# Kernel optimization log

Hardware: AMD Instinct MI355X
Metric: run time of the kernel (lower is better)

Reference implementation:

```python
import jax, jax.numpy as jnp
import numpy as np

BN_EPS = 1e-3  # Keras BatchNormalization default epsilon


def _conv_block(x, k):
    """Per-task conv (stride 2, pad 1) -> ReLU -> BatchNorm (center/scale=False, training).

    x: [B, E, H, W, Cin]  (B tasks, E examples per task)
    k: [B, kh, kw, Cin, Cout]  per-task kernel
    """
    def conv_one(xe, kt):  # xe: [E,H,W,Cin], kt: [kh,kw,Cin,Cout]
        return jax.lax.conv_general_dilated(
            xe, kt, window_strides=(2, 2), padding=[(1, 1), (1, 1)],
            dimension_numbers=('NHWC', 'HWIO', 'NHWC'))
    y = jax.nn.relu(jax.vmap(conv_one)(x, k))  # [B,E,H',W',Cout]
    # BatchNorm in training mode: moments over all axes except channels
    m = jnp.mean(y, axis=(0, 1, 2, 3))
    v = jnp.var(y, axis=(0, 1, 2, 3))
    return (y - m) * jax.lax.rsqrt(v + BN_EPS)


def setup_inputs() -> dict:
    key = jax.random.key(0)
    ks = jax.random.split(key, 6)
    B, E, H, C, O = 64, 64, 28, 64, 20
    return {
        'x': jax.random.normal(ks[0], (B, E, H, H, 1), dtype=jnp.float32),
        'k1': jax.random.normal(ks[1], (B, 3, 3, 1, C), dtype=jnp.float32) * 0.1,
        'k2': jax.random.normal(ks[2], (B, 3, 3, C, C), dtype=jnp.float32) * 0.05,
        'k3': jax.random.normal(ks[3], (B, 3, 3, C, C), dtype=jnp.float32) * 0.05,
        'k4': jax.random.normal(ks[4], (B, 3, 3, C, C), dtype=jnp.float32) * 0.05,
        'w_ro': jax.random.normal(ks[5], (B, C, O), dtype=jnp.float32) * 0.1,
    }


def reference(x, k1, k2, k3, k4, w_ro):
    h = _conv_block(x, k1)   # [B,E,14,14,C]
    h = _conv_block(h, k2)   # [B,E,7,7,C]
    h = _conv_block(h, k3)   # [B,E,4,4,C]
    h = _conv_block(h, k4)   # [B,E,2,2,C]
    # MaxPooling2D with pool size == full spatial extent -> global spatial max
    feat = jnp.max(h, axis=(2, 3))  # [B,E,C]
    # per-task readout matmul: [B,E,H] x [B,H,O] -> [B,E,O]
    return jnp.einsum('beh,bho->beo', feat, w_ro)
```

## Files before the change

### kernel.cpp

```cpp
#include <hip/hip_runtime.h>

#define BN_EPS 1e-3f

typedef __attribute__((ext_vector_type(8))) short bf16x8;
typedef __attribute__((ext_vector_type(16))) float floatx16;
typedef unsigned short u16;

__device__ __forceinline__ u16 f2bf(float f) {
  unsigned u = __float_as_uint(f);
  u += 0x7fffu + ((u >> 16) & 1u);
  return (u16)(u >> 16);
}
__device__ __forceinline__ float bf2f(u16 h) {
  return __uint_as_float(((unsigned)h) << 16);
}

static constexpr int NSHARD = 64;

__global__ __launch_bounds__(256) void conv1_k(
    const float* __restrict__ x, const float* __restrict__ k1,
    u16* __restrict__ y1, float* __restrict__ statsSh)
{
  __shared__ float xp[30 * 32];
  __shared__ float w1s[576];
  __shared__ float redsum[64], redss[64];

  const int be = blockIdx.x, b = be >> 6, tid = threadIdx.x;

  for (int i = tid; i < 960; i += 256) xp[i] = 0.f;
  for (int i = tid; i < 576; i += 256) w1s[i] = k1[(size_t)b * 576 + i];
  if (tid < 64) { redsum[tid] = 0.f; redss[tid] = 0.f; }
  __syncthreads();
  for (int i = tid; i < 784; i += 256) {
    const int r = i / 28, c = i - 28 * r;
    xp[(r + 1) * 32 + (c + 1)] = x[(size_t)be * 784 + i];
  }
  __syncthreads();

  if (tid < 224) {
    const int oy = tid >> 4, cg = (tid & 15) * 4;
    float w[4][9];
#pragma unroll
    for (int cc = 0; cc < 4; ++cc)
#pragma unroll
      for (int t = 0; t < 9; ++t) w[cc][t] = w1s[t * 64 + cg + cc];

    float xr[3][29];
#pragma unroll
    for (int ky = 0; ky < 3; ++ky)
#pragma unroll
      for (int j = 0; j < 29; ++j) xr[ky][j] = xp[(2 * oy + ky) * 32 + j];

    float sum[4] = {0.f, 0.f, 0.f, 0.f}, ss[4] = {0.f, 0.f, 0.f, 0.f};
#pragma unroll
    for (int ox = 0; ox < 14; ++ox) {
      alignas(8) u16 o[4];
#pragma unroll
      for (int cc = 0; cc < 4; ++cc) {
        float a = 0.f;
#pragma unroll
        for (int ky = 0; ky < 3; ++ky)
#pragma unroll
          for (int kx = 0; kx < 3; ++kx)
            a = fmaf(xr[ky][2 * ox + kx], w[cc][ky * 3 + kx], a);
        const float v = fmaxf(a, 0.f);
        o[cc] = f2bf(v);
        sum[cc] += v;
        ss[cc] = fmaf(v, v, ss[cc]);
      }
      *(uint2*)&y1[((size_t)be * 196 + oy * 14 + ox) * 64 + cg] = *(uint2*)o;
    }
#pragma unroll
    for (int cc = 0; cc < 4; ++cc) {
      atomicAdd(&redsum[cg + cc], sum[cc]);
      atomicAdd(&redss[cg + cc], ss[cc]);
    }
  }
  __syncthreads();
  if (tid < 64) {
    const int sh = be & (NSHARD - 1);
    atomicAdd(&statsSh[sh * 128 + tid], redsum[tid]);
    atomicAdd(&statsSh[sh * 128 + 64 + tid], redss[tid]);
  }
}

__global__ __launch_bounds__(256) void foldw_k(
    const float* __restrict__ W, const float* __restrict__ statsSh, float invN,
    u16* __restrict__ Wf, float* __restrict__ biasCls)
{
  __shared__ float T[64 * 68];
  __shared__ float P[256];
  __shared__ float s1[64], t1[64];
  __shared__ float tbS[64];

  const int b = blockIdx.x / 3, sg = blockIdx.x % 3;
  const int tid = threadIdx.x;

  {
    const int g = tid >> 7, cidx = tid & 127;
    float acc = 0.f;
    for (int k = 0; k < NSHARD / 2; ++k)
      acc += statsSh[(g * (NSHARD / 2) + k) * 128 + cidx];
    P[tid] = acc;
  }
  __syncthreads();
  if (tid < 64) {
    const float m = (P[tid] + P[tid + 128]) * invN;
    const float var = fmaf(-m, m, (P[64 + tid] + P[192 + tid]) * invN);
    const float s = rsqrtf(var + BN_EPS);
    s1[tid] = s;
    t1[tid] = -m * s;
  }
  __syncthreads();

  const int cin = tid >> 2, q0 = (tid & 3) * 16;
  const int cout = tid >> 2, ci0 = (tid & 3) * 16;
  for (int s = sg * 3; s < sg * 3 + 3; ++s) {
    if (tid < 64) tbS[tid] = 0.f;
    const float* ss = W + ((size_t)b * 9 + s) * 4096;
#pragma unroll
    for (int q = 0; q < 16; q += 4) {
      const float4 v = *(const float4*)(ss + cin * 64 + q0 + q);
      T[(q0 + q + 0) * 68 + cin] = v.x;
      T[(q0 + q + 1) * 68 + cin] = v.y;
      T[(q0 + q + 2) * 68 + cin] = v.z;
      T[(q0 + q + 3) * 68 + cin] = v.w;
    }
    __syncthreads();
    alignas(16) u16 tmp[16];
    float tb = 0.f;
#pragma unroll
    for (int j = 0; j < 16; ++j) {
      const float wv = T[cout * 68 + ci0 + j];
      tmp[j] = f2bf(wv * s1[ci0 + j]);
      tb = fmaf(t1[ci0 + j], wv, tb);
    }
    u16* dst = Wf + ((size_t)b * 9 + s) * 4096 + cout * 64 + ci0;
    *(uint4*)dst       = *(uint4*)&tmp[0];
    *(uint4*)(dst + 8) = *(uint4*)&tmp[8];
    atomicAdd(&tbS[cout], tb);
    __syncthreads();
    if (tid < 64) {
      const int ky = s / 3, kx = s % 3;
      const float tv = tbS[tid];
#pragma unroll
      for (int cls = 0; cls < 9; ++cls) {
        const int ry = cls / 3, rx = cls % 3;
        const bool valid = !((ry == 1 && ky == 0) || (ry == 2 && ky == 2) ||
                             (rx == 1 && kx == 0) || (rx == 2 && kx == 2));
        if (valid) atomicAdd(&biasCls[(size_t)b * 576 + cls * 64 + tid], tv);
      }
    }
    __syncthreads();
  }
}

template <int Hin, int Hout, int G>
__device__ __forceinline__ void conv_core(
    const u16* __restrict__ yin, const u16* __restrict__ Wf,
    const float* __restrict__ biasCls, u16* __restrict__ yout,
    float* __restrict__ statsSh, int blk)
{
  constexpr int PPI  = Hout * Hout;
  constexpr int ROWS = G * PPI;
  constexpr int BPT  = 64 / G;
  constexpr int MR   = G * Hin * Hin;
  constexpr int ZR   = MR;

  __shared__ __align__(16) u16 mapS[(MR + 1) * 72];
  __shared__ __align__(16) u16 Bb[2][64 * 72];
  __shared__ float biasS[576];
  __shared__ float redsum[64], redss[64];

  const int b = blk / BPT, e0 = (blk % BPT) * G;
  const int tid = threadIdx.x, lane = tid & 63, wave = tid >> 6;

  for (int i = tid; i < 576; i += 256) biasS[i] = biasCls[(size_t)b * 576 + i];
  if (tid < 64) { redsum[tid] = 0.f; redss[tid] = 0.f; }
  if (tid < 8) *(uint4*)&mapS[ZR * 72 + tid * 8] = uint4{0, 0, 0, 0};

  {
    const u16* src = yin + (size_t)(b * 64 + e0) * (Hin * Hin) * 64;
    for (int ch = tid; ch < MR * 8; ch += 256) {
      const int r = ch >> 3, c8 = ch & 7;
      *(uint4*)&mapS[r * 72 + c8 * 8] = *(const uint4*)(src + ch * 8);
    }
  }

  const int bco = tid >> 2, bci = (tid & 3) * 16;
  const u16* wb = Wf + (size_t)b * 9 * 4096 + bco * 64 + bci;
  {
    uint4 b0 = *(const uint4*)wb;
    uint4 b1 = *(const uint4*)(wb + 8);
    *(uint4*)&Bb[0][bco * 72 + bci]     = b0;
    *(uint4*)&Bb[0][bco * 72 + bci + 8] = b1;
  }

  const int m0 = (wave & 1) * 32, n0 = (wave >> 1) * 32;
  const int l31 = lane & 31, kq = (lane >> 5) * 8;
  const int lrow = m0 + l31;
  const bool rv = lrow < ROWS;
  const int img = rv ? lrow / PPI : 0;
  const int pp  = rv ? lrow % PPI : 0;
  const int oy = pp / Hout, ox = pp % Hout;

  floatx16 acc;
#pragma unroll
  for (int r = 0; r < 16; ++r) acc[r] = 0.f;

  __syncthreads();

#pragma unroll
  for (int s = 0; s < 9; ++s) {
    uint4 nb0, nb1;
    if (s < 8) {
      const u16* wsl = wb + (s + 1) * 4096;
      nb0 = *(const uint4*)wsl;
      nb1 = *(const uint4*)(wsl + 8);
    }
    const int ky = s / 3, kx = s % 3;
    int pix = ZR;
    if (rv) {
      const int iy = 2 * oy - 1 + ky, ix = 2 * ox - 1 + kx;
      if ((unsigned)iy < (unsigned)Hin && (unsigned)ix < (unsigned)Hin)
        pix = img * (Hin * Hin) + iy * Hin + ix;
    }
    const u16* ap = &mapS[pix * 72 + kq];
    const u16* bp = &Bb[s & 1][(n0 + l31) * 72 + kq];
#pragma unroll
    for (int kk = 0; kk < 4; ++kk) {
      bf16x8 a  = *(const bf16x8*)(ap + kk * 16);
      bf16x8 bv = *(const bf16x8*)(bp + kk * 16);
      acc = __builtin_amdgcn_mfma_f32_32x32x16_bf16(a, bv, acc, 0, 0, 0);
    }
    if (s < 8) {
      u16* d = &Bb[(s + 1) & 1][bco * 72 + bci];
      *(uint4*)d       = nb0;
      *(uint4*)(d + 8) = nb1;
    }
    __syncthreads();
  }

  const int col = n0 + l31;
  const int rb = m0 + 4 * (lane >> 5);
  float ls = 0.f, lss = 0.f;
#pragma unroll
  for (int r = 0; r < 16; ++r) {
    const int rw = rb + (r & 3) + 8 * (r >> 2);
    if (rw < ROWS) {
      const int re = rw / PPI, pr = rw % PPI;
      const int ooy = pr / Hout, oox = pr % Hout;
      const int ry = (ooy == 0) ? 1 : ((2 * ooy + 1 >= Hin) ? 2 : 0);
      const int rx = (oox == 0) ? 1 : ((2 * oox + 1 >= Hin) ? 2 : 0);
      const float v = fmaxf(acc[r] + biasS[(ry * 3 + rx) * 64 + col], 0.f);
      yout[((size_t)(b * 64 + e0 + re) * PPI + pr) * 64 + col] = f2bf(v);
      ls += v;
      lss = fmaf(v, v, lss);
    }
  }
  atomicAdd(&redsum[col], ls);
  atomicAdd(&redss[col], lss);
  __syncthreads();
  if (tid < 64) {
    const int sh = blk & (NSHARD - 1);
    atomicAdd(&statsSh[sh * 128 + tid], redsum[tid]);
    atomicAdd(&statsSh[sh * 128 + 64 + tid], redss[tid]);
  }
}

__global__ __launch_bounds__(256) void cg2_k(
    const u16* __restrict__ yin, const u16* __restrict__ Wf,
    const float* __restrict__ biasCls, u16* __restrict__ yout,
    float* __restrict__ statsSh) {
  conv_core<14, 7, 1>(yin, Wf, biasCls, yout, statsSh, blockIdx.x);
}
__global__ __launch_bounds__(256) void cg3_k(
    const u16* __restrict__ yin, const u16* __restrict__ Wf,
    const float* __restrict__ biasCls, u16* __restrict__ yout,
    float* __restrict__ statsSh) {
  conv_core<7, 4, 4>(yin, Wf, biasCls, yout, statsSh, blockIdx.x);
}
__global__ __launch_bounds__(256) void cg4_k(
    const u16* __restrict__ yin, const u16* __restrict__ Wf,
    const float* __restrict__ biasCls, u16* __restrict__ yout,
    float* __restrict__ statsSh) {
  conv_core<4, 2, 16>(yin, Wf, biasCls, yout, statsSh, blockIdx.x);
}

__global__ __launch_bounds__(256) void readout_k(
    const u16* __restrict__ y4, const float* __restrict__ w_ro,
    const float* __restrict__ statsSh, float invN, float* __restrict__ outp)
{
  __shared__ float wl[64 * 20];
  __shared__ float feat[64 * 64];
  __shared__ float P[256];
  __shared__ float sArr[64], tArr[64];

  const int b = blockIdx.x, tid = threadIdx.x;

  {
    const int g = tid >> 7, cidx = tid & 127;
    float acc = 0.f;
    for (int k = 0; k < NSHARD / 2; ++k)
      acc += statsSh[(g * (NSHARD / 2) + k) * 128 + cidx];
    P[tid] = acc;
  }
  for (int i = tid; i < 1280; i += 256) wl[i] = w_ro[(size_t)b * 1280 + i];
  __syncthreads();
  if (tid < 64) {
    const float m = (P[tid] + P[tid + 128]) * invN;
    const float var = fmaf(-m, m, (P[64 + tid] + P[192 + tid]) * invN);
    const float s = rsqrtf(var + BN_EPS);
    sArr[tid] = s;
    tArr[tid] = -m * s;
  }
  __syncthreads();

  {
    const int e = tid & 63;
    for (int c = tid >> 6; c < 64; c += 4) {
      const u16* p4 = y4 + ((size_t)(b * 64 + e) * 4) * 64 + c;
      const float v = fmaxf(fmaxf(bf2f(p4[0]), bf2f(p4[64])),
                            fmaxf(bf2f(p4[128]), bf2f(p4[192])));
      feat[c * 64 + e] = fmaf(v, sArr[c], tArr[c]);
    }
  }
  __syncthreads();

  const int e = tid >> 2, og = (tid & 3) * 5;
  float acc[5] = {0.f, 0.f, 0.f, 0.f, 0.f};
  for (int c = 0; c < 64; ++c) {
    const float f = feat[c * 64 + e];
#pragma unroll
    for (int j = 0; j < 5; ++j) acc[j] = fmaf(f, wl[c * 20 + og + j], acc[j]);
  }
#pragma unroll
  for (int j = 0; j < 5; ++j)
    outp[((size_t)b * 64 + e) * 20 + og + j] = acc[j];
}

extern "C" void kernel_launch(void* const* d_in, const int* in_sizes, int n_in,
                              void* d_out, int out_size, void* d_ws, size_t ws_size,
                              hipStream_t stream) {
  (void)in_sizes; (void)n_in; (void)out_size; (void)ws_size;
  const float* x   = (const float*)d_in[0];
  const float* k1  = (const float*)d_in[1];
  const float* k2  = (const float*)d_in[2];
  const float* k3  = (const float*)d_in[3];
  const float* k4  = (const float*)d_in[4];
  const float* wro = (const float*)d_in[5];
  float* out = (float*)d_out;
  char* ws = (char*)d_ws;

  float* stats = (float*)ws;
  float* bias2 = (float*)(ws + 131072);
  float* bias3 = bias2 + 36864;
  float* bias4 = bias3 + 36864;
  u16* k2f = (u16*)(ws + 131072 + 442368);
  u16* k3f = k2f + (size_t)2359296;
  u16* k4f = k3f + (size_t)2359296;
  u16* y2 = k4f + (size_t)2359296;
  u16* y1 = y2 + (size_t)12845056;
  u16* y3 = y1;
  u16* y4 = y3 + (size_t)4194304;

  float* st1 = stats;
  float* st2 = stats + 8192;
  float* st3 = stats + 16384;
  float* st4 = stats + 24576;

  hipMemsetAsync(stats, 0, 131072 + 442368, stream);

  conv1_k<<<4096, 256, 0, stream>>>(x, k1, y1, st1);
  foldw_k<<<192, 256, 0, stream>>>(k2, st1, 1.f / 802816.f, k2f, bias2);
  cg2_k<<<4096, 256, 0, stream>>>(y1, k2f, bias2, y2, st2);
  foldw_k<<<192, 256, 0, stream>>>(k3, st2, 1.f / 200704.f, k3f, bias3);
  cg3_k<<<1024, 256, 0, stream>>>(y2, k3f, bias3, y3, st3);
  foldw_k<<<192, 256, 0, stream>>>(k4, st3, 1.f / 65536.f, k4f, bias4);
  cg4_k<<<256, 256, 0, stream>>>(y3, k4f, bias4, y4, st4);
  readout_k<<<64, 256, 0, stream>>>(y4, wro, st4, 1.f / 16384.f, out);
}
```

Baseline: 265.3 us.

## Recompute conv1 inside conv2 kernel instead of materializing y1 activations

Conv1 now only computes BN statistics and no longer writes its bf16 output. A new fused conv2 kernel recomputes the conv1+ReLU output for one example directly into shared memory and feeds it to the MFMA conv2 path. This removes the global write and read of the large y1 tensor, at the cost of doing conv1 arithmetic twice. It also reworks the conv1 thread mapping to loop over pixels with all 256 threads.

```diff
diff --git a/kernel.cpp b/kernel.cpp
--- a/kernel.cpp
+++ b/kernel.cpp
@@ -17,64 +17,56 @@
 
 static constexpr int NSHARD = 64;
 
-__global__ __launch_bounds__(256) void conv1_k(
+__global__ __launch_bounds__(256) void conv1_stats_k(
     const float* __restrict__ x, const float* __restrict__ k1,
-    u16* __restrict__ y1, float* __restrict__ statsSh)
+    float* __restrict__ statsSh)
 {
-  __shared__ float xp[30 * 32];
+  __shared__ float xp[30 * 36];
   __shared__ float w1s[576];
   __shared__ float redsum[64], redss[64];
 
   const int be = blockIdx.x, b = be >> 6, tid = threadIdx.x;
 
-  for (int i = tid; i < 960; i += 256) xp[i] = 0.f;
+  for (int i = tid; i < 1080; i += 256) xp[i] = 0.f;
   for (int i = tid; i < 576; i += 256) w1s[i] = k1[(size_t)b * 576 + i];
   if (tid < 64) { redsum[tid] = 0.f; redss[tid] = 0.f; }
   __syncthreads();
   for (int i = tid; i < 784; i += 256) {
     const int r = i / 28, c = i - 28 * r;
-    xp[(r + 1) * 32 + (c + 1)] = x[(size_t)be * 784 + i];
-  }
-  __syncthreads();
-
-  if (tid < 224) {
-    const int oy = tid >> 4, cg = (tid & 15) * 4;
-    float w[4][9];
-#pragma unroll
-    for (int cc = 0; cc < 4; ++cc)
-#pragma unroll
-      for (int t = 0; t < 9; ++t) w[cc][t] = w1s[t * 64 + cg + cc];
-
-    float xr[3][29];
+    xp[(r + 1) * 36 + (c + 1)] = x[(size_t)be * 784 + i];
+  }
+  __syncthreads();
+
+  const int cg = (tid & 15) * 4, ps = tid >> 4;
+  float wreg[4][9];
+#pragma unroll
+  for (int cc = 0; cc < 4; ++cc)
+#pragma unroll
+    for (int t = 0; t < 9; ++t) wreg[cc][t] = w1s[t * 64 + cg + cc];
+
+  float sum[4] = {0.f, 0.f, 0.f, 0.f}, ss[4] = {0.f, 0.f, 0.f, 0.f};
+  for (int p = ps; p < 196; p += 16) {
+    const int iy = p / 14, ix = p - 14 * iy;
+    const float* xb = &xp[(2 * iy) * 36 + 2 * ix];
+    float xv[9];
 #pragma unroll
     for (int ky = 0; ky < 3; ++ky)
 #pragma unroll
-      for (int j = 0; j < 29; ++j) xr[ky][j] = xp[(2 * oy + ky) * 32 + j];
-
-    float sum[4] = {0.f, 0.f, 0.f, 0.f}, ss[4] = {0.f, 0.f, 0.f, 0.f};
-#pragma unroll
-    for (int ox = 0; ox < 14; ++ox) {
-      alignas(8) u16 o[4];
-#pragma unroll
-      for (int cc = 0; cc < 4; ++cc) {
-        float a = 0.f;
-#pragma unroll
-        for (int ky = 0; ky < 3; ++ky)
-#pragma unroll
-          for (int kx = 0; kx < 3; ++kx)
-            a = fmaf(xr[ky][2 * ox + kx], w[cc][ky * 3 + kx], a);
-        const float v = fmaxf(a, 0.f);
-        o[cc] = f2bf(v);
-        sum[cc] += v;
-        ss[cc] = fmaf(v, v, ss[cc]);
-      }
-      *(uint2*)&y1[((size_t)be * 196 + oy * 14 + ox) * 64 + cg] = *(uint2*)o;
-    }
+      for (int kx = 0; kx < 3; ++kx) xv[ky * 3 + kx] = xb[ky * 36 + kx];
 #pragma unroll
     for (int cc = 0; cc < 4; ++cc) {
-      atomicAdd(&redsum[cg + cc], sum[cc]);
-      atomicAdd(&redss[cg + cc], ss[cc]);
-    }
+      float a = 0.f;
+#pragma unroll
+      for (int t = 0; t < 9; ++t) a = fmaf(xv[t], wreg[cc][t], a);
+      const float v = fmaxf(a, 0.f);
+      sum[cc] += v;
+      ss[cc] = fmaf(v, v, ss[cc]);
+    }
+  }
+#pragma unroll
+  for (int cc = 0; cc < 4; ++cc) {
+    atomicAdd(&redsum[cg + cc], sum[cc]);
+    atomicAdd(&redss[cg + cc], ss[cc]);
   }
   __syncthreads();
   if (tid < 64) {
@@ -152,6 +144,143 @@
       }
     }
     __syncthreads();
+  }
+}
+
+__global__ __launch_bounds__(256) void cg2f_k(
+    const float* __restrict__ x, const float* __restrict__ k1,
+    const u16* __restrict__ k2f, const float* __restrict__ biasCls,
+    u16* __restrict__ y2, float* __restrict__ statsSh)
+{
+  __shared__ __align__(16) u16 mapS[197 * 72];
+  __shared__ __align__(16) char ov[2 * 8704];
+  __shared__ float biasS[576];
+  __shared__ float redsum[64], redss[64];
+
+  float* xp  = (float*)ov;
+  float* w1s = xp + 1080;
+  u16* Bb0 = (u16*)ov;
+  u16* Bb1 = (u16*)(ov + 8704);
+
+  const int be = blockIdx.x, b = be >> 6, tid = threadIdx.x;
+  const int lane = tid & 63, wave = tid >> 6;
+
+  for (int i = tid; i < 1080; i += 256) xp[i] = 0.f;
+  for (int i = tid; i < 576; i += 256) w1s[i] = k1[(size_t)b * 576 + i];
+  for (int i = tid; i < 576; i += 256) biasS[i] = biasCls[(size_t)b * 576 + i];
+  if (tid < 64) { redsum[tid] = 0.f; redss[tid] = 0.f; }
+  if (tid < 8) *(uint4*)&mapS[196 * 72 + tid * 8] = uint4{0, 0, 0, 0};
+  __syncthreads();
+  for (int i = tid; i < 784; i += 256) {
+    const int r = i / 28, c = i - 28 * r;
+    xp[(r + 1) * 36 + (c + 1)] = x[(size_t)be * 784 + i];
+  }
+  __syncthreads();
+
+  {
+    const int cg = (tid & 15) * 4, ps = tid >> 4;
+    float wreg[4][9];
+#pragma unroll
+    for (int cc = 0; cc < 4; ++cc)
+#pragma unroll
+      for (int t = 0; t < 9; ++t) wreg[cc][t] = w1s[t * 64 + cg + cc];
+
+    for (int p = ps; p < 196; p += 16) {
+      const int iy = p / 14, ix = p - 14 * iy;
+      const float* xb = &xp[(2 * iy) * 36 + 2 * ix];
+      float xv[9];
+#pragma unroll
+      for (int ky = 0; ky < 3; ++ky)
+#pragma unroll
+        for (int kx = 0; kx < 3; ++kx) xv[ky * 3 + kx] = xb[ky * 36 + kx];
+      alignas(8) u16 o[4];
+#pragma unroll
+      for (int cc = 0; cc < 4; ++cc) {
+        float a = 0.f;
+#pragma unroll
+        for (int t = 0; t < 9; ++t) a = fmaf(xv[t], wreg[cc][t], a);
+        o[cc] = f2bf(fmaxf(a, 0.f));
+      }
+      *(uint2*)&mapS[p * 72 + cg] = *(uint2*)o;
+    }
+  }
+  __syncthreads();
+
+  const int bco = tid >> 2, bci = (tid & 3) * 16;
+  const u16* wb = k2f + (size_t)b * 9 * 4096 + bco * 64 + bci;
+  {
+    uint4 b0 = *(const uint4*)wb;
+    uint4 b1 = *(const uint4*)(wb + 8);
+    *(uint4*)&Bb0[bco * 68 + bci]     = b0;
+    *(uint4*)&Bb0[bco * 68 + bci + 8] = b1;
+  }
+
+  const int m0 = (wave & 1) * 32, n0 = (wave >> 1) * 32;
+  const int l31 = lane & 31, kq = (lane >> 5) * 8;
+  const int lrow = m0 + l31;
+  const bool rv = lrow < 49;
+  const int oy = rv ? lrow / 7 : 0, ox = rv ? lrow % 7 : 0;
+
+  floatx16 acc;
+#pragma unroll
+  for (int r = 0; r < 16; ++r) acc[r] = 0.f;
+
+  __syncthreads();
+
+#pragma unroll
+  for (int s = 0; s < 9; ++s) {
+    uint4 nb0, nb1;
+    if (s < 8) {
+      const u16* wsl = wb + (s + 1) * 4096;
+      nb0 = *(const uint4*)wsl;
+      nb1 = *(const uint4*)(wsl + 8);
+    }
+    const int ky = s / 3, kx = s % 3;
+    int pix = 196;
+    if (rv) {
+      const int iy = 2 * oy - 1 + ky, ix = 2 * ox - 1 + kx;
+      if ((unsigned)iy < 14u && (unsigned)ix < 14u) pix = iy * 14 + ix;
+    }
+    const u16* ap = &mapS[pix * 72 + kq];
+    const u16* bp = (s & 1) ? &Bb1[(n0 + l31) * 68 + kq]
+                            : &Bb0[(n0 + l31) * 68 + kq];
+#pragma unroll
+    for (int kk = 0; kk < 4; ++kk) {
+      bf16x8 a  = *(const bf16x8*)(ap + kk * 16);
+      bf16x8 bv = *(const bf16x8*)(bp + kk * 16);
+      acc = __builtin_amdgcn_mfma_f32_32x32x16_bf16(a, bv, acc, 0, 0, 0);
+    }
+    if (s < 8) {
+      u16* d = ((s + 1) & 1) ? &Bb1[bco * 68 + bci] : &Bb0[bco * 68 + bci];
+      *(uint4*)d       = nb0;
+      *(uint4*)(d + 8) = nb1;
+    }
+    __syncthreads();
+  }
+
+  const int col = n0 + l31;
+  const int rb = m0 + 4 * (lane >> 5);
+  float ls = 0.f, lss = 0.f;
+#pragma unroll
+  for (int r = 0; r < 16; ++r) {
+    const int rw = rb + (r & 3) + 8 * (r >> 2);
+    if (rw < 49) {
+      const int ooy = rw / 7, oox = rw % 7;
+      const int ry = (ooy == 0) ? 1 : 0;
+      const int rx = (oox == 0) ? 1 : 0;
+      const float v = fmaxf(acc[r] + biasS[(ry * 3 + rx) * 64 + col], 0.f);
+      y2[((size_t)be * 49 + rw) * 64 + col] = f2bf(v);
+      ls += v;
+      lss = fmaf(v, v, lss);
+    }
+  }
+  atomicAdd(&redsum[col], ls);
+  atomicAdd(&redss[col], lss);
+  __syncthreads();
+  if (tid < 64) {
+    const int sh = be & (NSHARD - 1);
+    atomicAdd(&statsSh[sh * 128 + tid], redsum[tid]);
+    atomicAdd(&statsSh[sh * 128 + 64 + tid], redss[tid]);
   }
 }
 
@@ -268,12 +397,6 @@
   }
 }
 
-__global__ __launch_bounds__(256) void cg2_k(
-    const u16* __restrict__ yin, const u16* __restrict__ Wf,
-    const float* __restrict__ biasCls, u16* __restrict__ yout,
-    float* __restrict__ statsSh) {
-  conv_core<14, 7, 1>(yin, Wf, biasCls, yout, statsSh, blockIdx.x);
-}
 __global__ __launch_bounds__(256) void cg3_k(
     const u16* __restrict__ yin, const u16* __restrict__ Wf,
     const float* __restrict__ biasCls, u16* __restrict__ yout,
@@ -360,8 +483,7 @@
   u16* k3f = k2f + (size_t)2359296;
   u16* k4f = k3f + (size_t)2359296;
   u16* y2 = k4f + (size_t)2359296;
-  u16* y1 = y2 + (size_t)12845056;
-  u16* y3 = y1;
+  u16* y3 = y2 + (size_t)12845056;
   u16* y4 = y3 + (size_t)4194304;
 
   float* st1 = stats;
@@ -371,9 +493,9 @@
 
   hipMemsetAsync(stats, 0, 131072 + 442368, stream);
 
-  conv1_k<<<4096, 256, 0, stream>>>(x, k1, y1, st1);
+  conv1_stats_k<<<4096, 256, 0, stream>>>(x, k1, st1);
   foldw_k<<<192, 256, 0, stream>>>(k2, st1, 1.f / 802816.f, k2f, bias2);
-  cg2_k<<<4096, 256, 0, stream>>>(y1, k2f, bias2, y2, st2);
+  cg2f_k<<<4096, 256, 0, stream>>>(x, k1, k2f, bias2, y2, st2);
   foldw_k<<<192, 256, 0, stream>>>(k3, st2, 1.f / 200704.f, k3f, bias3);
   cg3_k<<<1024, 256, 0, stream>>>(y2, k3f, bias3, y3, st3);
   foldw_k<<<192, 256, 0, stream>>>(k4, st3, 1.f / 65536.f, k4f, bias4);
```

New measurement: 346.7 us. 30.7% more time.
